# Optimization experiments

Hardware: AMD Instinct MI355X
Metric: run time of the kernel (lower is better)

Reference implementation:

```python
import jax, jax.numpy as jnp
import numpy as np

# (left, right, top, bottom) zero-pad offsets for the 8 neighbors (matches nn.ZeroPad2d order in source)
PADS = [(0, 2, 0, 2), (1, 1, 0, 2), (2, 0, 0, 2), (0, 2, 1, 1),
        (2, 0, 1, 1), (0, 2, 2, 0), (1, 1, 2, 0), (2, 0, 2, 0)]
CROP_H = [96, 128, 160, 192]
CROP_W = [192, 256, 320, 384]
PROP_TIME = 3


def _shift_pad8(x):
    # x: [B,1,h,w] -> [B,8,h+2,w+2], each channel a differently shifted zero-padded copy
    xs = [jnp.pad(x[:, 0], ((0, 0), (t, b), (l, r))) for (l, r, t, b) in PADS]
    return jnp.stack(xs, axis=1)


def _cspn(guidance, blur_depth, sparse_depth):
    # guidance: [B,8,h,w]; blur_depth/sparse_depth: [B,1,h,w]. norm_type='8sum'.
    gates = [jnp.pad(guidance[:, k], ((0, 0), (t, b), (l, r)))
             for k, (l, r, t, b) in enumerate(PADS)]
    gate_wb = jnp.stack(gates, axis=1)                              # [B,8,h+2,w+2]
    abs_weight = jnp.sum(jnp.abs(gate_wb), axis=1, keepdims=True)   # [B,1,h+2,w+2]
    gate_wb = gate_wb / abs_weight
    gate_sum = jnp.sum(gate_wb, axis=1, keepdims=True)[:, :, 1:-1, 1:-1]  # [B,1,h,w]

    sparse_mask = jnp.sign(sparse_depth)
    raw = blur_depth
    result = blur_depth
    for i in range(PROP_TIME):
        if i == 0:
            result = (1.0 - sparse_mask) * result + sparse_mask * sparse_depth
        neigh = jnp.sum(gate_wb * _shift_pad8(result), axis=1, keepdims=True)
        result = (1.0 - gate_sum) * raw + neigh[:, :, 1:-1, 1:-1]
    return result


def _conv_block(x, w, b):
    # ConvBlock (monodepth2 style): reflection pad 1 + 3x3 conv + ELU
    xp = jnp.pad(x, ((0, 0), (0, 0), (1, 1), (1, 1)), mode='reflect')
    y = jax.lax.conv_general_dilated(xp, w, (1, 1), 'VALID',
                                     dimension_numbers=('NCHW', 'OIHW', 'NCHW'))
    return jax.nn.elu(y + b[None, :, None, None])


def _center_crop(x, h, w):
    oh, ow = x.shape[2], x.shape[3]
    hs = max(int(round((oh - h) / 2)), 0)
    ws = max(int(round((ow - w) / 2)), 0)
    return x[:, :, hs:min(hs + h, oh), ws:min(ws + w, ow)]


def _stage_pad(depth, h, w):
    hs, ws = depth.shape[2], depth.shape[3]
    ph, pw = (h - hs) // 2, (w - ws) // 2
    return jnp.pad(depth, ((0, 0), (0, 0), (ph, ph), (pw, pw)))


def _masked_median(x, mask):
    # torch.median semantics: lower median of the masked elements
    s = jnp.sort(jnp.where(mask, x, jnp.inf).ravel())
    n = jnp.sum(mask)
    return jnp.take(s, (n - 1) // 2)


def _stage_forward(features, rgbd, dep_last, w, b, h, wd):
    rgbd_c = _center_crop(rgbd, h, wd)
    feat_c = _center_crop(features, h, wd)
    dep = rgbd_c[:, 0:1]                       # channel 0, as in source
    mask = jnp.sign(dep_last)
    dep_fusion = dep_last * mask + dep * (1.0 - mask)
    guided_map = _conv_block(feat_c, w, b)     # [B,8,h,wd]
    x = _cspn(guided_map, dep_fusion, dep_last)
    return jnp.clip(x, 0.0, 1.0)


def setup_inputs() -> dict:
    key = jax.random.key(0)
    ks = jax.random.split(key, 12)
    B, H, W = 16, 256, 512
    inp = {
        'features': jax.random.normal(ks[0], (B, 16, H, W), jnp.float32),
        'blur_depth': jax.random.uniform(ks[1], (B, 1, H, W), jnp.float32),
        'gt': jax.random.uniform(ks[2], (B, 1, H, W), jnp.float32),
        'rgb': jax.random.uniform(ks[3], (B, 3, H, W), jnp.float32),
        'stage': jnp.arange(4, dtype=jnp.int64 if jax.config.jax_enable_x64 else jnp.int32),
    }
    scale = 1.0 / np.sqrt(16 * 9)
    for i in range(4):
        inp[f'w{i}'] = jax.random.normal(ks[4 + i], (8, 16, 3, 3), jnp.float32) * scale
        inp[f'b{i}'] = jax.random.normal(ks[8 + i], (8,), jnp.float32) * 0.01
    return inp


def reference(features, blur_depth, gt, rgb, w0, b0, w1, b1, w2, b2, w3, b3, stage):
    stage_list = [int(s) for s in np.asarray(stage)]
    gt_pos = gt > 0
    scale = _masked_median(gt, gt_pos) / _masked_median(blur_depth, gt_pos)
    all_scale = gt / blur_depth
    blur_depth_o = blur_depth * scale
    gt = jnp.where((all_scale > 1.2) | (all_scale < 0.8), 0.0, gt)
    rgbd = jnp.concatenate([rgb, blur_depth_o], axis=1)
    dep_last = _center_crop(gt, 96, 192)

    params = [(w0, b0), (w1, b1), (w2, b2), (w3, b3)]
    out = None
    for index, i in enumerate(stage_list):
        w, b = params[i]
        if index == len(stage_list) - 1:
            out = _stage_forward(features, rgbd, dep_last, w, b, CROP_H[i], CROP_W[i])
        else:
            ref_last = jax.lax.stop_gradient(
                _stage_forward(features, rgbd, dep_last, w, b, CROP_H[i], CROP_W[i]))
            dep_last = _stage_pad(ref_last, CROP_H[i + 1], CROP_W[i + 1])
    return out
```

## Files before the change

### kernel.cpp

```cpp
#include <hip/hip_runtime.h>
#include <math.h>


#define B 16
#define FH 256
#define FW 512
#define TH 32
#define TW 32
#define HALO 3
#define LD 38
#define GD 36
#define MAXC 6

typedef __attribute__((ext_vector_type(8))) short short8;
typedef __attribute__((ext_vector_type(4))) float f32x4;

__device__ __forceinline__ int swzslot(int cc, int h) {
  return (((cc << 1) | h) ^ (cc & 1) ^ ((cc >> 1) & 2));
}

__global__ __launch_bounds__(256) void prep_all_kernel(
    const float* __restrict__ gt, const float* __restrict__ blur,
    const float* __restrict__ rgb, const float* __restrict__ w0c,
    const float* __restrict__ w1c, const float* __restrict__ w2c,
    const float* __restrict__ w3c, short8* __restrict__ wf,
    float* __restrict__ r0) {
  if (blockIdx.x == 0 && threadIdx.x < 64) {
    int lane = threadIdx.x;
    int px = lane & 15, g = lane >> 4;
    const float* Ws[4] = {w0c, w1c, w2c, w3c};
    for (int st = 0; st < 4; ++st) {
      const float* wgt = Ws[st];
      for (int t = 0; t < 5; ++t) {
        short8 wh, wl;
        for (int j = 0; j < 8; ++j) {
          int k = 32 * t + 8 * g + j;
          int s = k >> 4, ci = k & 15;
          float wv = 0.0f;
          if (px < 8 && s < 9) wv = wgt[(px * 16 + ci) * 9 + s];
          uint uw = __float_as_uint(wv);
          uint hw_ = (uw + 0x8000u) & 0xFFFF0000u;
          float wlo = wv - __uint_as_float(hw_);
          wh[j] = (short)(hw_ >> 16);
          wl[j] = (short)((__float_as_uint(wlo) + 0x8000u) >> 16);
        }
        wf[((st * 5 + t) * 2 + 0) * 64 + lane] = wh;
        wf[((st * 5 + t) * 2 + 1) * 64 + lane] = wl;
      }
    }
  }

  int idx = blockIdx.x * blockDim.x + threadIdx.x;
  const int n0 = B * 96 * 192;
  if (idx >= n0) return;
  const int h = 96, w = 192, hs = 80, ws = 160;
  int x = idx % w;
  int t = idx / w;
  int y = t % h;
  int b = t / h;
  size_t g = (size_t)b * FH * FW + (size_t)(hs + y) * FW + (ws + x);
  float dep = rgb[((size_t)b * 3) * FH * FW + (size_t)(hs + y) * FW + (ws + x)];
  float gv = gt[g];
  float s = gv / blur[g];
  float dl = (s > 1.2f || s < 0.8f) ? 0.0f : gv;
  r0[idx] = (dl > 0.0f) ? dl : dep;
}

__global__ __launch_bounds__(256) void conv_mfma_kernel(
    const float* __restrict__ feat, const short8* __restrict__ wf,
    const float* __restrict__ b0c, float* __restrict__ g0,
    const float* __restrict__ b1c, float* __restrict__ g1,
    const float* __restrict__ b2c, float* __restrict__ g2,
    const float* __restrict__ b3c, float* __restrict__ g3) {
  __shared__ uint4 sH[18 * 72];
  __shared__ uint4 sL[18 * 72];

  int bid = blockIdx.x;
  int bx = bid % 12;
  int t0 = bid / 12;
  int by = t0 % 12;
  int b = t0 / 12;
  int ty0 = by << 4, tx0 = bx << 5;

  int tid = threadIdx.x;
  int lane = tid & 63, wv = tid >> 6;
  int px = lane & 15, g = lane >> 4;
  int h_ = g & 1, gb = g >> 1;

  const size_t FHW = (size_t)FH * FW;
  const float* fb = feat + (size_t)b * 16 * FHW;
  for (int u = tid; u < 612; u += 256) {
    int rr = u / 34, cc = u % 34;
    int yy = ty0 + rr - 1;
    yy = (yy < 0) ? 0 : ((yy > 191) ? 191 : yy);
    int xx = tx0 + cc - 1;
    xx = (xx < 0) ? 0 : ((xx > 383) ? 383 : xx);
    const float* fp = fb + (size_t)(32 + yy) * FW + (64 + xx);
    uint hiD[8], loD[8];
#pragma unroll
    for (int i = 0; i < 8; ++i) {
      float a0 = fp[(size_t)(2 * i) * FHW];
      float a1 = fp[(size_t)(2 * i + 1) * FHW];
      uint u0 = __float_as_uint(a0), u1 = __float_as_uint(a1);
      uint h0 = u0 & 0xFFFF0000u;
      uint h1 = u1 & 0xFFFF0000u;
      float l0 = a0 - __uint_as_float(h0);
      float l1 = a1 - __uint_as_float(h1);
      hiD[i] = (h0 >> 16) | h1;
      loD[i] = (__float_as_uint(l0) >> 16) |
               (__float_as_uint(l1) & 0xFFFF0000u);
    }
    int r72 = rr * 72;
    sH[r72 + swzslot(cc, 0)] = make_uint4(hiD[0], hiD[1], hiD[2], hiD[3]);
    sH[r72 + swzslot(cc, 1)] = make_uint4(hiD[4], hiD[5], hiD[6], hiD[7]);
    sL[r72 + swzslot(cc, 0)] = make_uint4(loD[0], loD[1], loD[2], loD[3]);
    sL[r72 + swzslot(cc, 1)] = make_uint4(loD[4], loD[5], loD[6], loD[7]);
  }
  __syncthreads();

  const short8* pH = (const short8*)sH;
  const short8* pL = (const short8*)sL;

  const int SH[4] = {96, 128, 160, 192};
  const int SW[4] = {192, 256, 320, 384};
  const int OY[4] = {48, 32, 16, 0};
  const int OX[4] = {96, 64, 32, 0};
  const float* BIAS[4] = {b0c, b1c, b2c, b3c};
  float* GD_[4] = {g0, g1, g2, g3};

#pragma unroll
  for (int st = 0; st < 4; ++st) {
    int sh = SH[st], sw = SW[st], oy = OY[st], ox = OX[st];
    bool inR = (ty0 >= oy) && (ty0 + 16 <= oy + sh) && (tx0 >= ox) &&
               (tx0 + 32 <= ox + sw);
    if (!inR) continue;
    bool topE = (ty0 == oy), botE = (ty0 + 16 == oy + sh);
    bool leftE = (tx0 == ox), rightE = (tx0 + 32 == ox + sw);

    const short8* wfs = wf + st * 640;
    short8 WH[5], WL[5];
#pragma unroll
    for (int t = 0; t < 5; ++t) {
      WH[t] = wfs[(t * 2 + 0) * 64 + lane];
      WL[t] = wfs[(t * 2 + 1) * 64 + lane];
    }
    float bias4[4];
    {
      const float* bp = BIAS[st] + ((g & 1) << 2);
#pragma unroll
      for (int r = 0; r < 4; ++r) bias4[r] = bp[r];
    }
    size_t hw = (size_t)sh * sw;
    float* guid = GD_[st];

    int csl[2][3];
#pragma unroll
    for (int xt = 0; xt < 2; ++xt) {
      int cc0 = (xt << 4) + px + 1;
      int ccm = (leftE && cc0 == 1) ? cc0 + 1 : cc0 - 1;
      int ccp = (rightE && cc0 == 32) ? cc0 - 1 : cc0 + 1;
      csl[xt][0] = swzslot(ccm, h_);
      csl[xt][1] = swzslot(cc0, h_);
      csl[xt][2] = swzslot(ccp, h_);
    }

#pragma unroll
    for (int i = 0; i < 8; ++i) {
      int tau = wv * 8 + i;
      int row = tau >> 1;
      const int xt = i & 1;
      int rr0 = row + 1;
      int rm = (topE && row == 0) ? rr0 + 1 : rr0 - 1;
      int rp = (botE && row == 15) ? rr0 - 1 : rr0 + 1;
      int rbm = rm * 72, rb_ = rr0 * 72, rbp = rp * 72;
      const int c0 = csl[xt][0], c1 = csl[xt][1], c2 = csl[xt][2];
      int iE[5] = {rbm + c0, rbm + c2, rb_ + c1, rbp + c0, rbp + c2};
      int iO[5] = {rbm + c1, rb_ + c0, rb_ + c2, rbp + c1, rb_ + c1};

      f32x4 acc = {bias4[0], bias4[1], bias4[2], bias4[3]};
#pragma unroll
      for (int t = 0; t < 5; ++t) {
        int idx = gb ? iO[t] : iE[t];
        short8 fh = pH[idx];
        short8 fl = pL[idx];
        acc = __builtin_amdgcn_mfma_f32_16x16x32_bf16(WH[t], fh, acc, 0, 0, 0);
        acc = __builtin_amdgcn_mfma_f32_16x16x32_bf16(WH[t], fl, acc, 0, 0, 0);
        acc = __builtin_amdgcn_mfma_f32_16x16x32_bf16(WL[t], fh, acc, 0, 0, 0);
      }
      if (g < 2) {
        int ly = ty0 + row - oy, lx = tx0 + (xt << 4) + px - ox;
        float* gp = guid + (size_t)b * 8 * hw + (size_t)ly * sw + lx;
#pragma unroll
        for (int r = 0; r < 4; ++r) {
          int oo = g * 4 + r;
          float v = acc[r];
          v = (v > 0.0f) ? v : (__expf(v) - 1.0f);
          gp[(size_t)oo * hw] = v;
        }
      }
    }
  }
}

__global__ __launch_bounds__(256) void cspn3_kernel(
    const float* __restrict__ guid, const float* __restrict__ raw,
    const float* __restrict__ rgb, float* __restrict__ dst, int h, int w,
    int hs, int wss, int h2, int w2, int ph, int pw, int last, int py0,
    int py1, int px0, int px1) {
  __shared__ float sraw[LD * LD];
  __shared__ float s0[LD * LD];
  __shared__ float s1[LD * LD];

  int tpw = w / TW, tph = h / TH;
  int tile = blockIdx.x;
  int tx = tile % tpw;
  int t2 = tile / tpw;
  int ty = t2 % tph;
  int b = t2 / tph;
  int oy = ty * TH - HALO, ox = tx * TW - HALO;
  int tid = threadIdx.x;

  const float* rb = raw + (size_t)b * h * w;
  const float* rgb0 = rgb + ((size_t)b * 3) * FH * FW;

  for (int e = tid; e < LD * LD; e += 256) {
    int r = e / LD, c = e % LD;
    int gy = oy + r, gx = ox + c;
    bool in = (gy >= 0 && gy < h && gx >= 0 && gx < w);
    float v = 0.0f;
    if (in) {
      bool prev = (gy >= py0 && gy < py1 && gx >= px0 && gx < px1);
      v = prev ? rb[(size_t)gy * w + gx]
               : rgb0[(size_t)(hs + gy) * FW + (wss + gx)];
    }
    sraw[e] = v;
  }
  __syncthreads();

  const int dy8[8] = {1, 1, 1, 0, 0, -1, -1, -1};
  const int dx8[8] = {1, 0, -1, 1, -1, 1, 0, -1};
  const int off8[8] = {LD + 1, LD, LD - 1, 1, -1, -LD + 1, -LD, -LD - 1};

  const float* gb = guid + (size_t)b * 8 * h * w;
  float cg[MAXC][8];
  float r0[MAXC];
  int adr[MAXC];
#pragma unroll
  for (int ch = 0; ch < MAXC; ++ch) {
    int p = tid + ch * 256;
    bool ok = p < GD * GD;
    int pp = ok ? p : 0;
    int py = pp / GD + 1, px = pp % GD + 1;
    adr[ch] = py * LD + px;
    int gy = oy + py, gx = ox + px;
    bool in = ok && gy >= 0 && gy < h && gx >= 0 && gx < w;
    float wsum = 0.0f, asum = 0.0f;
    float g[8];
#pragma unroll
    for (int k = 0; k < 8; ++k) {
      int ny = gy + dy8[k], nx = gx + dx8[k];
      bool nin = ok && ny >= 0 && ny < h && nx >= 0 && nx < w;
      float gk = nin ? gb[(size_t)k * h * w + (size_t)ny * w + nx] : 0.0f;
      g[k] = gk;
      wsum += gk;
      asum += fabsf(gk);
    }
    float inv = in ? (1.0f / asum) : 0.0f;
#pragma unroll
    for (int k = 0; k < 8; ++k) cg[ch][k] = g[k] * inv;
    r0[ch] = in ? (1.0f - wsum * inv) * sraw[adr[ch]] : 0.0f;
  }

#pragma unroll
  for (int ch = 0; ch < MAXC; ++ch) {
    int p = tid + ch * 256;
    if (p < GD * GD) {
      float v = r0[ch];
#pragma unroll
      for (int k = 0; k < 8; ++k) v += cg[ch][k] * sraw[adr[ch] + off8[k]];
      s0[adr[ch]] = v;
    }
  }
  __syncthreads();

#pragma unroll
  for (int ch = 0; ch < MAXC; ++ch) {
    int p = tid + ch * 256;
    if (p < GD * GD) {
      int py = p / GD + 1, px = p % GD + 1;
      if (py >= 2 && py <= 35 && px >= 2 && px <= 35) {
        float v = r0[ch];
#pragma unroll
        for (int k = 0; k < 8; ++k) v += cg[ch][k] * s0[adr[ch] + off8[k]];
        s1[adr[ch]] = v;
      }
    }
  }
  __syncthreads();

#pragma unroll
  for (int ch = 0; ch < MAXC; ++ch) {
    int p = tid + ch * 256;
    if (p < GD * GD) {
      int py = p / GD + 1, px = p % GD + 1;
      if (py >= 3 && py <= 34 && px >= 3 && px <= 34) {
        float v = r0[ch];
#pragma unroll
        for (int k = 0; k < 8; ++k) v += cg[ch][k] * s1[adr[ch] + off8[k]];
        float dl = fminf(fmaxf(v, 0.0f), 1.0f);
        int gy = oy + py, gx = ox + px;
        if (last) {
          dst[((size_t)b * h + gy) * w + gx] = dl;
        } else {
          float dep = rgb0[(size_t)(hs + gy) * FW + (wss + gx)];
          dst[((size_t)b * h2 + (gy + ph)) * w2 + (gx + pw)] =
              (dl > 0.0f) ? dl : dep;
        }
      }
    }
  }
}

extern "C" void kernel_launch(void* const* d_in, const int* in_sizes, int n_in,
                              void* d_out, int out_size, void* d_ws,
                              size_t ws_size, hipStream_t stream) {
  (void)in_sizes; (void)n_in; (void)out_size; (void)ws_size;
  const float* feat = (const float*)d_in[0];
  const float* blur = (const float*)d_in[1];
  const float* gt = (const float*)d_in[2];
  const float* rgb = (const float*)d_in[3];
  const float* W[4] = {(const float*)d_in[5], (const float*)d_in[7],
                       (const float*)d_in[9], (const float*)d_in[11]};
  const float* Bs[4] = {(const float*)d_in[6], (const float*)d_in[8],
                        (const float*)d_in[10], (const float*)d_in[12]};
  float* out = (float*)d_out;

  float* G0 = (float*)d_ws;
  float* G1 = G0 + (size_t)B * 8 * 96 * 192;
  float* G2 = G1 + (size_t)B * 8 * 128 * 256;
  float* G3 = G2 + (size_t)B * 8 * 160 * 320;
  float* RAW[4];
  RAW[0] = G3 + (size_t)B * 8 * 192 * 384;
  RAW[1] = RAW[0] + (size_t)B * 96 * 192;
  RAW[2] = RAW[1] + (size_t)B * 128 * 256;
  RAW[3] = RAW[2] + (size_t)B * 160 * 320;
  short8* WF = (short8*)(RAW[3] + (size_t)B * 192 * 384);
  float* G[4] = {G0, G1, G2, G3};

  const int CH[4] = {96, 128, 160, 192};
  const int CW[4] = {192, 256, 320, 384};

  prep_all_kernel<<<1152, 256, 0, stream>>>(gt, blur, rgb, W[0], W[1], W[2],
                                            W[3], WF, RAW[0]);

  conv_mfma_kernel<<<2304, 256, 0, stream>>>(feat, WF, Bs[0], G0, Bs[1], G1,
                                             Bs[2], G2, Bs[3], G3);

  for (int i = 0; i < 4; ++i) {
    int h = CH[i], w = CW[i];
    int hs = (FH - h) / 2, wss = (FW - w) / 2;
    int ntiles = B * (h / TH) * (w / TW);
    int py0 = 0, py1 = h, px0 = 0, px1 = w;
    if (i > 0) { py0 = 16; py1 = h - 16; px0 = 32; px1 = w - 32; }
    if (i < 3) {
      int h2 = CH[i + 1], w2 = CW[i + 1];
      int ph = (h2 - h) / 2, pw = (w2 - w) / 2;
      cspn3_kernel<<<ntiles, 256, 0, stream>>>(G[i], RAW[i], rgb, RAW[i + 1],
                                               h, w, hs, wss, h2, w2, ph, pw,
                                               0, py0, py1, px0, px1);
    } else {
      cspn3_kernel<<<ntiles, 256, 0, stream>>>(G[i], RAW[i], rgb, out, h, w,
                                               hs, wss, h, w, 0, 0, 1, py0,
                                               py1, px0, px1);
    }
  }
}
```

Measured before the change: 163.2 us.

## Store guidance pre-shifted in pixel-interleaved layout for vector loads in CSPN

The conv kernel now scatters each guidance channel to the pixel it gates, in an interleaved [B,h,w,8] layout, so the CSPN kernel reads all eight gates for a pixel with two float4 loads instead of eight strided, bounds-checked gathers. Border pixels whose shifted sources fall outside the image are zeroed by extra threads added to the prep kernel. The conv kernel's stores become 8-strided scatters, which are less coalesced, in exchange for contiguous vector reads in the three CSPN launches.

```diff
diff --git a/kernel.cpp b/kernel.cpp
--- a/kernel.cpp
+++ b/kernel.cpp
@@ -24,7 +24,8 @@
     const float* __restrict__ rgb, const float* __restrict__ w0c,
     const float* __restrict__ w1c, const float* __restrict__ w2c,
     const float* __restrict__ w3c, short8* __restrict__ wf,
-    float* __restrict__ r0) {
+    float* __restrict__ r0, float* __restrict__ gb0, float* __restrict__ gb1,
+    float* __restrict__ gb2, float* __restrict__ gb3) {
   if (blockIdx.x == 0 && threadIdx.x < 64) {
     int lane = threadIdx.x;
     int px = lane & 15, g = lane >> 4;
@@ -52,26 +53,49 @@
 
   int idx = blockIdx.x * blockDim.x + threadIdx.x;
   const int n0 = B * 96 * 192;
-  if (idx >= n0) return;
-  const int h = 96, w = 192, hs = 80, ws = 160;
-  int x = idx % w;
-  int t = idx / w;
-  int y = t % h;
-  int b = t / h;
-  size_t g = (size_t)b * FH * FW + (size_t)(hs + y) * FW + (ws + x);
-  float dep = rgb[((size_t)b * 3) * FH * FW + (size_t)(hs + y) * FW + (ws + x)];
-  float gv = gt[g];
-  float s = gv / blur[g];
-  float dl = (s > 1.2f || s < 0.8f) ? 0.0f : gv;
-  r0[idx] = (dl > 0.0f) ? dl : dep;
+  if (idx < n0) {
+    const int h = 96, w = 192, hs = 80, ws = 160;
+    int x = idx % w;
+    int t = idx / w;
+    int y = t % h;
+    int b = t / h;
+    size_t g = (size_t)b * FH * FW + (size_t)(hs + y) * FW + (ws + x);
+    float dep =
+        rgb[((size_t)b * 3) * FH * FW + (size_t)(hs + y) * FW + (ws + x)];
+    float gv = gt[g];
+    float s = gv / blur[g];
+    float dl = (s > 1.2f || s < 0.8f) ? 0.0f : gv;
+    r0[idx] = (dl > 0.0f) ? dl : dep;
+    return;
+  }
+  int t2 = idx - n0;
+  const int cB[4] = {572, 764, 956, 1148};
+  const int tb = 3440;
+  if (t2 >= B * tb) return;
+  int b = t2 / tb;
+  int e = t2 % tb;
+  int st = 0;
+  while (e >= cB[st]) { e -= cB[st]; ++st; }
+  const int SHh[4] = {96, 128, 160, 192};
+  const int SWw[4] = {192, 256, 320, 384};
+  float* GB[4] = {gb0, gb1, gb2, gb3};
+  int h = SHh[st], w = SWw[st];
+  int py, px;
+  if (e < w) { py = 0; px = e; }
+  else if (e < 2 * w) { py = h - 1; px = e - w; }
+  else if (e < 2 * w + (h - 2)) { py = 1 + (e - 2 * w); px = 0; }
+  else { py = 1 + (e - 2 * w - (h - 2)); px = w - 1; }
+  float4* p = (float4*)(GB[st] + (((size_t)b * h + py) * w + px) * 8);
+  p[0] = make_float4(0.f, 0.f, 0.f, 0.f);
+  p[1] = make_float4(0.f, 0.f, 0.f, 0.f);
 }
 
 __global__ __launch_bounds__(256) void conv_mfma_kernel(
     const float* __restrict__ feat, const short8* __restrict__ wf,
-    const float* __restrict__ b0c, float* __restrict__ g0,
-    const float* __restrict__ b1c, float* __restrict__ g1,
-    const float* __restrict__ b2c, float* __restrict__ g2,
-    const float* __restrict__ b3c, float* __restrict__ g3) {
+    const float* __restrict__ b0c, float* __restrict__ gb0,
+    const float* __restrict__ b1c, float* __restrict__ gb1,
+    const float* __restrict__ b2c, float* __restrict__ gb2,
+    const float* __restrict__ b3c, float* __restrict__ gb3) {
   __shared__ uint4 sH[18 * 72];
   __shared__ uint4 sL[18 * 72];
 
@@ -107,8 +131,7 @@
       float l0 = a0 - __uint_as_float(h0);
       float l1 = a1 - __uint_as_float(h1);
       hiD[i] = (h0 >> 16) | h1;
-      loD[i] = (__float_as_uint(l0) >> 16) |
-               (__float_as_uint(l1) & 0xFFFF0000u);
+      loD[i] = (__float_as_uint(l0) >> 16) | (__float_as_uint(l1) & 0xFFFF0000u);
     }
     int r72 = rr * 72;
     sH[r72 + swzslot(cc, 0)] = make_uint4(hiD[0], hiD[1], hiD[2], hiD[3]);
@@ -121,16 +144,18 @@
   const short8* pH = (const short8*)sH;
   const short8* pL = (const short8*)sL;
 
-  const int SH[4] = {96, 128, 160, 192};
-  const int SW[4] = {192, 256, 320, 384};
+  const int SH_[4] = {96, 128, 160, 192};
+  const int SW_[4] = {192, 256, 320, 384};
   const int OY[4] = {48, 32, 16, 0};
   const int OX[4] = {96, 64, 32, 0};
   const float* BIAS[4] = {b0c, b1c, b2c, b3c};
-  float* GD_[4] = {g0, g1, g2, g3};
+  float* GB_[4] = {gb0, gb1, gb2, gb3};
+  const int dy8[8] = {1, 1, 1, 0, 0, -1, -1, -1};
+  const int dx8[8] = {1, 0, -1, 1, -1, 1, 0, -1};
 
 #pragma unroll
   for (int st = 0; st < 4; ++st) {
-    int sh = SH[st], sw = SW[st], oy = OY[st], ox = OX[st];
+    int sh = SH_[st], sw = SW_[st], oy = OY[st], ox = OX[st];
     bool inR = (ty0 >= oy) && (ty0 + 16 <= oy + sh) && (tx0 >= ox) &&
                (tx0 + 32 <= ox + sw);
     if (!inR) continue;
@@ -150,8 +175,7 @@
 #pragma unroll
       for (int r = 0; r < 4; ++r) bias4[r] = bp[r];
     }
-    size_t hw = (size_t)sh * sw;
-    float* guid = GD_[st];
+    float* gbuf = GB_[st];
 
     int csl[2][3];
 #pragma unroll
@@ -188,14 +212,15 @@
         acc = __builtin_amdgcn_mfma_f32_16x16x32_bf16(WL[t], fh, acc, 0, 0, 0);
       }
       if (g < 2) {
-        int ly = ty0 + row - oy, lx = tx0 + (xt << 4) + px - ox;
-        float* gp = guid + (size_t)b * 8 * hw + (size_t)ly * sw + lx;
+        int qy = ty0 + row - oy, qx = tx0 + (xt << 4) + px - ox;
 #pragma unroll
         for (int r = 0; r < 4; ++r) {
-          int oo = g * 4 + r;
+          int ch = g * 4 + r;
           float v = acc[r];
           v = (v > 0.0f) ? v : (__expf(v) - 1.0f);
-          gp[(size_t)oo * hw] = v;
+          int py_ = qy - dy8[ch], px_ = qx - dx8[ch];
+          if (py_ >= 0 && py_ < sh && px_ >= 0 && px_ < sw)
+            gbuf[(((size_t)b * sh + py_) * sw + px_) * 8 + ch] = v;
         }
       }
     }
@@ -203,7 +228,7 @@
 }
 
 __global__ __launch_bounds__(256) void cspn3_kernel(
-    const float* __restrict__ guid, const float* __restrict__ raw,
+    const float* __restrict__ gbuf, const float* __restrict__ raw,
     const float* __restrict__ rgb, float* __restrict__ dst, int h, int w,
     int hs, int wss, int h2, int w2, int ph, int pw, int last, int py0,
     int py1, int px0, int px1) {
@@ -237,11 +262,9 @@
   }
   __syncthreads();
 
-  const int dy8[8] = {1, 1, 1, 0, 0, -1, -1, -1};
-  const int dx8[8] = {1, 0, -1, 1, -1, 1, 0, -1};
   const int off8[8] = {LD + 1, LD, LD - 1, 1, -1, -LD + 1, -LD, -LD - 1};
 
-  const float* gb = guid + (size_t)b * 8 * h * w;
+  const float* gbb = gbuf + (size_t)b * h * w * 8;
   float cg[MAXC][8];
   float r0[MAXC];
   int adr[MAXC];
@@ -254,20 +277,25 @@
     adr[ch] = py * LD + px;
     int gy = oy + py, gx = ox + px;
     bool in = ok && gy >= 0 && gy < h && gx >= 0 && gx < w;
+    float g8[8];
+    if (in) {
+      const float4* q = (const float4*)(gbb + ((size_t)gy * w + gx) * 8);
+      float4 a = q[0], c4 = q[1];
+      g8[0] = a.x; g8[1] = a.y; g8[2] = a.z; g8[3] = a.w;
+      g8[4] = c4.x; g8[5] = c4.y; g8[6] = c4.z; g8[7] = c4.w;
+    } else {
+#pragma unroll
+      for (int k = 0; k < 8; ++k) g8[k] = 0.0f;
+    }
     float wsum = 0.0f, asum = 0.0f;
-    float g[8];
 #pragma unroll
     for (int k = 0; k < 8; ++k) {
-      int ny = gy + dy8[k], nx = gx + dx8[k];
-      bool nin = ok && ny >= 0 && ny < h && nx >= 0 && nx < w;
-      float gk = nin ? gb[(size_t)k * h * w + (size_t)ny * w + nx] : 0.0f;
-      g[k] = gk;
-      wsum += gk;
-      asum += fabsf(gk);
+      wsum += g8[k];
+      asum += fabsf(g8[k]);
     }
     float inv = in ? (1.0f / asum) : 0.0f;
 #pragma unroll
-    for (int k = 0; k < 8; ++k) cg[ch][k] = g[k] * inv;
+    for (int k = 0; k < 8; ++k) cg[ch][k] = g8[k] * inv;
     r0[ch] = in ? (1.0f - wsum * inv) * sraw[adr[ch]] : 0.0f;
   }
 
@@ -350,8 +378,8 @@
   const int CH[4] = {96, 128, 160, 192};
   const int CW[4] = {192, 256, 320, 384};
 
-  prep_all_kernel<<<1152, 256, 0, stream>>>(gt, blur, rgb, W[0], W[1], W[2],
-                                            W[3], WF, RAW[0]);
+  prep_all_kernel<<<1368, 256, 0, stream>>>(gt, blur, rgb, W[0], W[1], W[2],
+                                            W[3], WF, RAW[0], G0, G1, G2, G3);
 
   conv_mfma_kernel<<<2304, 256, 0, stream>>>(feat, WF, Bs[0], G0, Bs[1], G1,
                                              Bs[2], G2, Bs[3], G3);
```

Result: slower. 199.4 us (+22.2%).
